# Performance work log

Measured on AMD Instinct MI355X. Metric: run time of the kernel, lower is better.

## Reference

```python
import jax, jax.numpy as jnp
import numpy as np

LOTRI2MAT = np.array([[0, 1, 3], [1, 2, 4], [3, 4, 5]])  # lower-tri 6-vec -> symmetric 3x3
MAT2LOTRI_I = np.array([0, 1, 1, 2, 2, 2])
MAT2LOTRI_J = np.array([0, 0, 1, 0, 1, 2])


def trilinear_warp_border(img, ddf):
    """MONAI Warp(mode='bilinear', padding_mode='border', align_corners=True).
    img: (B,C,H,W,D), ddf: (B,3,H,W,D) displacement in voxel units.
    Samples img at x + ddf(x), clamping coords to the volume (border padding).
    """
    B, C, H, W, D = img.shape
    base = jnp.stack(
        jnp.meshgrid(jnp.arange(H), jnp.arange(W), jnp.arange(D), indexing='ij'),
        axis=0,
    ).astype(img.dtype)  # (3,H,W,D)
    coords = ddf + base[None]  # (B,3,H,W,D)
    x = jnp.clip(coords[:, 0], 0.0, H - 1)
    y = jnp.clip(coords[:, 1], 0.0, W - 1)
    z = jnp.clip(coords[:, 2], 0.0, D - 1)

    x0f, y0f, z0f = jnp.floor(x), jnp.floor(y), jnp.floor(z)
    fx, fy, fz = x - x0f, y - y0f, z - z0f
    x0 = jnp.clip(x0f.astype(jnp.int32), 0, H - 1)
    y0 = jnp.clip(y0f.astype(jnp.int32), 0, W - 1)
    z0 = jnp.clip(z0f.astype(jnp.int32), 0, D - 1)
    x1 = jnp.minimum(x0 + 1, H - 1)
    y1 = jnp.minimum(y0 + 1, W - 1)
    z1 = jnp.minimum(z0 + 1, D - 1)

    def gather(img_b, xi, yi, zi):
        flat = (xi * W + yi) * D + zi  # (H,W,D)
        return img_b.reshape(C, -1)[:, flat.reshape(-1)].reshape(C, H, W, D)

    g = jax.vmap(gather)  # over batch

    out = jnp.zeros_like(img)
    for xi, wx in ((x0, 1.0 - fx), (x1, fx)):
        for yi, wy in ((y0, 1.0 - fy), (y1, fy)):
            for zi, wz in ((z0, 1.0 - fz), (z1, fz)):
                out = out + g(img, xi, yi, zi) * (wx * wy * wz)[:, None]
    return out


def jacobian_of_ddf(ddf):
    """J = I + du/dx via central differences (one-sided at boundaries).
    ddf: (B,3,H,W,D) -> (B,H,W,D,3,3) with J[...,i,j] = d u_i / d x_j + delta_ij."""
    grads = jnp.gradient(ddf, axis=(2, 3, 4))  # list over j of (B,3,H,W,D)
    J = jnp.stack(grads, axis=2)  # (B,3(i),3(j),H,W,D)
    J = J + jnp.eye(3, dtype=ddf.dtype)[None, :, :, None, None, None]
    return jnp.transpose(J, (0, 3, 4, 5, 1, 2))  # (B,H,W,D,3,3)


def setup_inputs() -> dict:
    key = jax.random.key(0)
    k1, k2 = jax.random.split(key)
    dti = jax.random.normal(k1, (2, 6, 64, 64, 64), dtype=jnp.float32)
    ddf = jax.random.normal(k2, (2, 3, 64, 64, 64), dtype=jnp.float32)
    return {"dti": dti, "ddf": ddf}


def reference(dti, ddf):
    b, _, h, w, d = dti.shape
    # 1) trilinear warp of the 6-channel lower-tri DTI
    dti_warped = trilinear_warp_border(dti, ddf)  # (B,6,H,W,D)
    # 2) lower-tri -> full symmetric 3x3, spatial-last
    M = dti_warped[:, LOTRI2MAT]                      # (B,3,3,H,W,D)
    M = jnp.transpose(M, (0, 3, 4, 5, 1, 2))          # (B,H,W,D,3,3)
    # 3) Jacobian of the deformation and its polar-decomposition rotation (finite strain)
    J = jacobian_of_ddf(ddf)                          # (B,H,W,D,3,3)
    U, _, Vh = jnp.linalg.svd(J, full_matrices=False)
    R = jnp.matmul(U, Vh)                             # orthogonal factor of J
    # 4) rotate tensors: R^T M R
    out = jnp.einsum('...ji,...jk,...kl->...il', R, M, R)
    # 5) back to lower-tri channel-first form
    out = jnp.transpose(out, (0, 4, 5, 1, 2, 3))      # (B,3,3,H,W,D)
    return out[:, MAT2LOTRI_I, MAT2LOTRI_J]           # (B,6,H,W,D)
```

## Files before the change

### kernel.cpp

```cpp
#include <hip/hip_runtime.h>

#define NVOX 262144
#define TOTAL (2 * NVOX)

__global__ __launch_bounds__(256)
void warpdti_kernel(const float* __restrict__ dti,
                    const float* __restrict__ ddf,
                    float* __restrict__ out)
{
    const int idx = blockIdx.x * 256 + threadIdx.x;
    const int b = idx >> 18;
    const int r = idx & (NVOX - 1);
    const int x = r >> 12;
    const int y = (r >> 6) & 63;
    const int z = r & 63;

    const float* db = ddf + (size_t)b * 3 * NVOX;

    const float ux = db[r];
    const float uy = db[NVOX + r];
    const float uz = db[2 * NVOX + r];

    const float cx = fminf(fmaxf((float)x + ux, 0.0f), 63.0f);
    const float cy = fminf(fmaxf((float)y + uy, 0.0f), 63.0f);
    const float cz = fminf(fmaxf((float)z + uz, 0.0f), 63.0f);
    const float fx0 = floorf(cx), fy0 = floorf(cy), fz0 = floorf(cz);
    const float fx = cx - fx0, fy = cy - fy0, fz = cz - fz0;
    const int x0 = (int)fx0, y0 = (int)fy0, z0 = (int)fz0;
    const int x1 = min(x0 + 1, 63), y1 = min(y0 + 1, 63), z1 = min(z0 + 1, 63);

    const float gx = 1.0f - fx, gy = 1.0f - fy, gz = 1.0f - fz;
    const float w000 = gx * gy * gz, w001 = gx * gy * fz;
    const float w010 = gx * fy * gz, w011 = gx * fy * fz;
    const float w100 = fx * gy * gz, w101 = fx * gy * fz;
    const float w110 = fx * fy * gz, w111 = fx * fy * fz;

    const int o000 = (x0 * 64 + y0) * 64 + z0, o001 = (x0 * 64 + y0) * 64 + z1;
    const int o010 = (x0 * 64 + y1) * 64 + z0, o011 = (x0 * 64 + y1) * 64 + z1;
    const int o100 = (x1 * 64 + y0) * 64 + z0, o101 = (x1 * 64 + y0) * 64 + z1;
    const int o110 = (x1 * 64 + y1) * 64 + z0, o111 = (x1 * 64 + y1) * 64 + z1;

    const float* tb = dti + (size_t)b * 6 * NVOX;
    float m[6];
#pragma unroll
    for (int c = 0; c < 6; ++c) {
        const float* tc = tb + c * NVOX;
        m[c] = w000 * tc[o000] + w001 * tc[o001]
             + w010 * tc[o010] + w011 * tc[o011]
             + w100 * tc[o100] + w101 * tc[o101]
             + w110 * tc[o110] + w111 * tc[o111];
    }

    const int xm = max(x - 1, 0), xp = min(x + 1, 63);
    const int ym = max(y - 1, 0), yp = min(y + 1, 63);
    const int zm = max(z - 1, 0), zp = min(z + 1, 63);
    const float sx = (xp - xm == 2) ? 0.5f : 1.0f;
    const float sy = (yp - ym == 2) ? 0.5f : 1.0f;
    const float sz = (zp - zm == 2) ? 0.5f : 1.0f;

    const float uc0 = ux, uc1 = uy, uc2 = uz;
    float P[3][3];
#pragma unroll
    for (int i = 0; i < 3; ++i) {
        const float* ui = db + i * NVOX;
        const float ctr = (i == 0) ? uc0 : (i == 1) ? uc1 : uc2;
        P[i][0] = (ui[(xp * 64 + y) * 64 + z] - ui[(xm * 64 + y) * 64 + z]) * sx
                + (i == 0 ? 1.0f : 0.0f);
        P[i][1] = (ui[(x * 64 + yp) * 64 + z] - ui[(x * 64 + ym) * 64 + z]) * sy
                + (i == 1 ? 1.0f : 0.0f);
        P[i][2] = (__shfl(ctr, zp) - __shfl(ctr, zm)) * sz + (i == 2 ? 1.0f : 0.0f);
    }

    float cond_est = 0.0f;
#pragma unroll
    for (int it = 0; it < 8; ++it) {
        const float C00 = P[1][1] * P[2][2] - P[1][2] * P[2][1];
        const float C01 = P[1][2] * P[2][0] - P[1][0] * P[2][2];
        const float C02 = P[1][0] * P[2][1] - P[1][1] * P[2][0];
        const float C10 = P[0][2] * P[2][1] - P[0][1] * P[2][2];
        const float C11 = P[0][0] * P[2][2] - P[0][2] * P[2][0];
        const float C12 = P[0][1] * P[2][0] - P[0][0] * P[2][1];
        const float C20 = P[0][1] * P[1][2] - P[0][2] * P[1][1];
        const float C21 = P[0][2] * P[1][0] - P[0][0] * P[1][2];
        const float C22 = P[0][0] * P[1][1] - P[0][1] * P[1][0];
        const float det = P[0][0] * C00 + P[0][1] * C01 + P[0][2] * C02;

        const float n2 = P[0][0]*P[0][0] + P[0][1]*P[0][1] + P[0][2]*P[0][2]
                       + P[1][0]*P[1][0] + P[1][1]*P[1][1] + P[1][2]*P[1][2]
                       + P[2][0]*P[2][0] + P[2][1]*P[2][1] + P[2][2]*P[2][2];
        const float a2 = C00*C00 + C01*C01 + C02*C02
                       + C10*C10 + C11*C11 + C12*C12
                       + C20*C20 + C21*C21 + C22*C22;

        const float ad = fmaxf(fabsf(det), 1e-30f);
        if (it == 0) cond_est = sqrtf(n2 * a2) / ad;

        const float t  = fmaxf(sqrtf(a2 / n2), 1e-20f);
        const float sg = (det < 0.0f) ? -1.0f : 1.0f;
        const float c1 = 0.5f * sqrtf(t / ad);
        const float c2 = 0.5f * sg / sqrtf(t * ad);

        P[0][0] = c1 * P[0][0] + c2 * C00;  P[0][1] = c1 * P[0][1] + c2 * C01;  P[0][2] = c1 * P[0][2] + c2 * C02;
        P[1][0] = c1 * P[1][0] + c2 * C10;  P[1][1] = c1 * P[1][1] + c2 * C11;  P[1][2] = c1 * P[1][2] + c2 * C12;
        P[2][0] = c1 * P[2][0] + c2 * C20;  P[2][1] = c1 * P[2][1] + c2 * C21;  P[2][2] = c1 * P[2][2] + c2 * C22;
    }

    if (cond_est > 1e4f) {
        double X[3][3];
#pragma unroll
        for (int i = 0; i < 3; ++i) {
            const float* ui = db + i * NVOX;
            X[i][0] = ((double)ui[(xp * 64 + y) * 64 + z]
                     - (double)ui[(xm * 64 + y) * 64 + z]) * (double)sx + (i == 0 ? 1.0 : 0.0);
            X[i][1] = ((double)ui[(x * 64 + yp) * 64 + z]
                     - (double)ui[(x * 64 + ym) * 64 + z]) * (double)sy + (i == 1 ? 1.0 : 0.0);
            X[i][2] = ((double)ui[(x * 64 + y) * 64 + zp]
                     - (double)ui[(x * 64 + y) * 64 + zm]) * (double)sz + (i == 2 ? 1.0 : 0.0);
        }
        for (int it = 0; it < 14; ++it) {
            double mx = 0.0;
#pragma unroll
            for (int i = 0; i < 3; ++i)
#pragma unroll
                for (int j = 0; j < 3; ++j) mx = fmax(mx, fabs(X[i][j]));
            const double s = 1.0 / fmax(mx, 1e-300);
#pragma unroll
            for (int i = 0; i < 3; ++i)
#pragma unroll
                for (int j = 0; j < 3; ++j) X[i][j] *= s;

            const double C00 = X[1][1] * X[2][2] - X[1][2] * X[2][1];
            const double C01 = X[1][2] * X[2][0] - X[1][0] * X[2][2];
            const double C02 = X[1][0] * X[2][1] - X[1][1] * X[2][0];
            const double C10 = X[0][2] * X[2][1] - X[0][1] * X[2][2];
            const double C11 = X[0][0] * X[2][2] - X[0][2] * X[2][0];
            const double C12 = X[0][1] * X[2][0] - X[0][0] * X[2][1];
            const double C20 = X[0][1] * X[1][2] - X[0][2] * X[1][1];
            const double C21 = X[0][2] * X[1][0] - X[0][0] * X[1][2];
            const double C22 = X[0][0] * X[1][1] - X[0][1] * X[1][0];
            const double det = X[0][0] * C00 + X[0][1] * C01 + X[0][2] * C02;

            const double n2 = X[0][0]*X[0][0] + X[0][1]*X[0][1] + X[0][2]*X[0][2]
                            + X[1][0]*X[1][0] + X[1][1]*X[1][1] + X[1][2]*X[1][2]
                            + X[2][0]*X[2][0] + X[2][1]*X[2][1] + X[2][2]*X[2][2];
            const double a2 = C00*C00 + C01*C01 + C02*C02
                            + C10*C10 + C11*C11 + C12*C12
                            + C20*C20 + C21*C21 + C22*C22;

            const double t  = fmax(sqrt(a2 / n2), 1e-150);
            const double ad = fmax(fabs(det), 1e-280);
            const double sg = (det < 0.0) ? -1.0 : 1.0;
            const double c1 = 0.5 * sqrt(t / ad);
            const double c2 = 0.5 * sg / sqrt(t * ad);

            X[0][0] = c1 * X[0][0] + c2 * C00;  X[0][1] = c1 * X[0][1] + c2 * C01;  X[0][2] = c1 * X[0][2] + c2 * C02;
            X[1][0] = c1 * X[1][0] + c2 * C10;  X[1][1] = c1 * X[1][1] + c2 * C11;  X[1][2] = c1 * X[1][2] + c2 * C12;
            X[2][0] = c1 * X[2][0] + c2 * C20;  X[2][1] = c1 * X[2][1] + c2 * C21;  X[2][2] = c1 * X[2][2] + c2 * C22;
        }
#pragma unroll
        for (int i = 0; i < 3; ++i)
#pragma unroll
            for (int j = 0; j < 3; ++j) P[i][j] = (float)X[i][j];
    }

    const float M3[3][3] = {{m[0], m[1], m[3]},
                            {m[1], m[2], m[4]},
                            {m[3], m[4], m[5]}};
    float T[3][3];
#pragma unroll
    for (int i = 0; i < 3; ++i)
#pragma unroll
        for (int j = 0; j < 3; ++j)
            T[i][j] = P[0][i] * M3[0][j] + P[1][i] * M3[1][j] + P[2][i] * M3[2][j];

    float A[3][3];
#pragma unroll
    for (int i = 0; i < 3; ++i)
#pragma unroll
        for (int j = 0; j < 3; ++j)
            A[i][j] = T[i][0] * P[0][j] + T[i][1] * P[1][j] + T[i][2] * P[2][j];

    float* ob = out + (size_t)b * 6 * NVOX;
    ob[0 * NVOX + r] = A[0][0];
    ob[1 * NVOX + r] = A[1][0];
    ob[2 * NVOX + r] = A[1][1];
    ob[3 * NVOX + r] = A[2][0];
    ob[4 * NVOX + r] = A[2][1];
    ob[5 * NVOX + r] = A[2][2];
}

extern "C" void kernel_launch(void* const* d_in, const int* in_sizes, int n_in,
                              void* d_out, int out_size, void* d_ws, size_t ws_size,
                              hipStream_t stream) {
    const float* dti = (const float*)d_in[0];
    const float* ddf = (const float*)d_in[1];
    float* out = (float*)d_out;
    warpdti_kernel<<<TOTAL / 256, 256, 0, stream>>>(dti, ddf, out);
}
```

Measured before the change: 113.7 us.

## Defer ill-conditioned voxels to a double-precision rescue kernel and pair z-loads

The rare fp64 polar-decomposition fallback moves out of the main kernel. Flagged voxels are appended to a workspace list with an atomic counter, and a small second kernel recomputes them in double precision. This removes divergence and register pressure from the main kernel. The trilinear gather also loads the two z-neighbours as one 2-float vector, and the fp32 Newton iterations drop from 8 to 6. In exchange the change adds two extra launches, an atomic per flagged voxel and a cap of 8192 rescued voxels, and the fewer iterations may lose accuracy on moderately conditioned voxels.

```diff
diff --git a/kernel.cpp b/kernel.cpp
--- a/kernel.cpp
+++ b/kernel.cpp
@@ -3,10 +3,17 @@
 #define NVOX 262144
 #define TOTAL (2 * NVOX)
 
+typedef float f2u __attribute__((ext_vector_type(2), aligned(4)));
+
+__global__ void zero_count(int* __restrict__ bad) {
+    if (threadIdx.x == 0) bad[0] = 0;
+}
+
 __global__ __launch_bounds__(256)
-void warpdti_kernel(const float* __restrict__ dti,
-                    const float* __restrict__ ddf,
-                    float* __restrict__ out)
+void warp_main(const float* __restrict__ dti,
+               const float* __restrict__ ddf,
+               float* __restrict__ out,
+               int* __restrict__ bad, int max_bad)
 {
     const int idx = blockIdx.x * 256 + threadIdx.x;
     const int b = idx >> 18;
@@ -27,28 +34,30 @@
     const float fx0 = floorf(cx), fy0 = floorf(cy), fz0 = floorf(cz);
     const float fx = cx - fx0, fy = cy - fy0, fz = cz - fz0;
     const int x0 = (int)fx0, y0 = (int)fy0, z0 = (int)fz0;
-    const int x1 = min(x0 + 1, 63), y1 = min(y0 + 1, 63), z1 = min(z0 + 1, 63);
+    const int x1 = min(x0 + 1, 63), y1 = min(y0 + 1, 63);
 
     const float gx = 1.0f - fx, gy = 1.0f - fy, gz = 1.0f - fz;
-    const float w000 = gx * gy * gz, w001 = gx * gy * fz;
-    const float w010 = gx * fy * gz, w011 = gx * fy * fz;
-    const float w100 = fx * gy * gz, w101 = fx * gy * fz;
-    const float w110 = fx * fy * gz, w111 = fx * fy * fz;
-
-    const int o000 = (x0 * 64 + y0) * 64 + z0, o001 = (x0 * 64 + y0) * 64 + z1;
-    const int o010 = (x0 * 64 + y1) * 64 + z0, o011 = (x0 * 64 + y1) * 64 + z1;
-    const int o100 = (x1 * 64 + y0) * 64 + z0, o101 = (x1 * 64 + y0) * 64 + z1;
-    const int o110 = (x1 * 64 + y1) * 64 + z0, o111 = (x1 * 64 + y1) * 64 + z1;
+    const float q00 = gx * gy, q01 = gx * fy, q10 = fx * gy, q11 = fx * fy;
+
+    const bool ztop = (z0 == 63);
+    const int zb = ztop ? 62 : z0;
+    const int p00 = (x0 * 64 + y0) * 64 + zb, p01 = (x0 * 64 + y1) * 64 + zb;
+    const int p10 = (x1 * 64 + y0) * 64 + zb, p11 = (x1 * 64 + y1) * 64 + zb;
 
     const float* tb = dti + (size_t)b * 6 * NVOX;
     float m[6];
 #pragma unroll
     for (int c = 0; c < 6; ++c) {
         const float* tc = tb + c * NVOX;
-        m[c] = w000 * tc[o000] + w001 * tc[o001]
-             + w010 * tc[o010] + w011 * tc[o011]
-             + w100 * tc[o100] + w101 * tc[o101]
-             + w110 * tc[o110] + w111 * tc[o111];
+        const f2u v00 = *(const f2u*)(tc + p00);
+        const f2u v01 = *(const f2u*)(tc + p01);
+        const f2u v10 = *(const f2u*)(tc + p10);
+        const f2u v11 = *(const f2u*)(tc + p11);
+        const float l00 = (ztop ? v00.y : v00.x) * gz + v00.y * fz;
+        const float l01 = (ztop ? v01.y : v01.x) * gz + v01.y * fz;
+        const float l10 = (ztop ? v10.y : v10.x) * gz + v10.y * fz;
+        const float l11 = (ztop ? v11.y : v11.x) * gz + v11.y * fz;
+        m[c] = q00 * l00 + q01 * l01 + q10 * l10 + q11 * l11;
     }
 
     const int xm = max(x - 1, 0), xp = min(x + 1, 63);
@@ -58,12 +67,11 @@
     const float sy = (yp - ym == 2) ? 0.5f : 1.0f;
     const float sz = (zp - zm == 2) ? 0.5f : 1.0f;
 
-    const float uc0 = ux, uc1 = uy, uc2 = uz;
     float P[3][3];
 #pragma unroll
     for (int i = 0; i < 3; ++i) {
         const float* ui = db + i * NVOX;
-        const float ctr = (i == 0) ? uc0 : (i == 1) ? uc1 : uc2;
+        const float ctr = (i == 0) ? ux : (i == 1) ? uy : uz;
         P[i][0] = (ui[(xp * 64 + y) * 64 + z] - ui[(xm * 64 + y) * 64 + z]) * sx
                 + (i == 0 ? 1.0f : 0.0f);
         P[i][1] = (ui[(x * 64 + yp) * 64 + z] - ui[(x * 64 + ym) * 64 + z]) * sy
@@ -73,7 +81,7 @@
 
     float cond_est = 0.0f;
 #pragma unroll
-    for (int it = 0; it < 8; ++it) {
+    for (int it = 0; it < 6; ++it) {
         const float C00 = P[1][1] * P[2][2] - P[1][2] * P[2][1];
         const float C01 = P[1][2] * P[2][0] - P[1][0] * P[2][2];
         const float C02 = P[1][0] * P[2][1] - P[1][1] * P[2][0];
@@ -105,64 +113,6 @@
         P[2][0] = c1 * P[2][0] + c2 * C20;  P[2][1] = c1 * P[2][1] + c2 * C21;  P[2][2] = c1 * P[2][2] + c2 * C22;
     }
 
-    if (cond_est > 1e4f) {
-        double X[3][3];
-#pragma unroll
-        for (int i = 0; i < 3; ++i) {
-            const float* ui = db + i * NVOX;
-            X[i][0] = ((double)ui[(xp * 64 + y) * 64 + z]
-                     - (double)ui[(xm * 64 + y) * 64 + z]) * (double)sx + (i == 0 ? 1.0 : 0.0);
-            X[i][1] = ((double)ui[(x * 64 + yp) * 64 + z]
-                     - (double)ui[(x * 64 + ym) * 64 + z]) * (double)sy + (i == 1 ? 1.0 : 0.0);
-            X[i][2] = ((double)ui[(x * 64 + y) * 64 + zp]
-                     - (double)ui[(x * 64 + y) * 64 + zm]) * (double)sz + (i == 2 ? 1.0 : 0.0);
-        }
-        for (int it = 0; it < 14; ++it) {
-            double mx = 0.0;
-#pragma unroll
-            for (int i = 0; i < 3; ++i)
-#pragma unroll
-                for (int j = 0; j < 3; ++j) mx = fmax(mx, fabs(X[i][j]));
-            const double s = 1.0 / fmax(mx, 1e-300);
-#pragma unroll
-            for (int i = 0; i < 3; ++i)
-#pragma unroll
-                for (int j = 0; j < 3; ++j) X[i][j] *= s;
-
-            const double C00 = X[1][1] * X[2][2] - X[1][2] * X[2][1];
-            const double C01 = X[1][2] * X[2][0] - X[1][0] * X[2][2];
-            const double C02 = X[1][0] * X[2][1] - X[1][1] * X[2][0];
-            const double C10 = X[0][2] * X[2][1] - X[0][1] * X[2][2];
-            const double C11 = X[0][0] * X[2][2] - X[0][2] * X[2][0];
-            const double C12 = X[0][1] * X[2][0] - X[0][0] * X[2][1];
-            const double C20 = X[0][1] * X[1][2] - X[0][2] * X[1][1];
-            const double C21 = X[0][2] * X[1][0] - X[0][0] * X[1][2];
-            const double C22 = X[0][0] * X[1][1] - X[0][1] * X[1][0];
-            const double det = X[0][0] * C00 + X[0][1] * C01 + X[0][2] * C02;
-
-            const double n2 = X[0][0]*X[0][0] + X[0][1]*X[0][1] + X[0][2]*X[0][2]
-                            + X[1][0]*X[1][0] + X[1][1]*X[1][1] + X[1][2]*X[1][2]
-                            + X[2][0]*X[2][0] + X[2][1]*X[2][1] + X[2][2]*X[2][2];
-            const double a2 = C00*C00 + C01*C01 + C02*C02
-                            + C10*C10 + C11*C11 + C12*C12
-                            + C20*C20 + C21*C21 + C22*C22;
-
-            const double t  = fmax(sqrt(a2 / n2), 1e-150);
-            const double ad = fmax(fabs(det), 1e-280);
-            const double sg = (det < 0.0) ? -1.0 : 1.0;
-            const double c1 = 0.5 * sqrt(t / ad);
-            const double c2 = 0.5 * sg / sqrt(t * ad);
-
-            X[0][0] = c1 * X[0][0] + c2 * C00;  X[0][1] = c1 * X[0][1] + c2 * C01;  X[0][2] = c1 * X[0][2] + c2 * C02;
-            X[1][0] = c1 * X[1][0] + c2 * C10;  X[1][1] = c1 * X[1][1] + c2 * C11;  X[1][2] = c1 * X[1][2] + c2 * C12;
-            X[2][0] = c1 * X[2][0] + c2 * C20;  X[2][1] = c1 * X[2][1] + c2 * C21;  X[2][2] = c1 * X[2][2] + c2 * C22;
-        }
-#pragma unroll
-        for (int i = 0; i < 3; ++i)
-#pragma unroll
-            for (int j = 0; j < 3; ++j) P[i][j] = (float)X[i][j];
-    }
-
     const float M3[3][3] = {{m[0], m[1], m[3]},
                             {m[1], m[2], m[4]},
                             {m[3], m[4], m[5]}};
@@ -187,6 +137,117 @@
     ob[3 * NVOX + r] = A[2][0];
     ob[4 * NVOX + r] = A[2][1];
     ob[5 * NVOX + r] = A[2][2];
+
+    if (cond_est > 1e4f) {
+        const int slot = atomicAdd(bad, 1);
+        if (slot < max_bad) bad[1 + slot] = idx;
+    }
+}
+
+__global__ __launch_bounds__(256)
+void rescue(const float* __restrict__ dti,
+            const float* __restrict__ ddf,
+            float* __restrict__ out,
+            const int* __restrict__ bad, int max_bad)
+{
+    const int n = min(bad[0], max_bad);
+    for (int k = blockIdx.x * 256 + threadIdx.x; k < n; k += 4 * 256) {
+        const int idx = bad[1 + k];
+        const int b = idx >> 18;
+        const int r = idx & (NVOX - 1);
+        const int x = r >> 12;
+        const int y = (r >> 6) & 63;
+        const int z = r & 63;
+
+        const float* db = ddf + (size_t)b * 3 * NVOX;
+
+        const float cx = fminf(fmaxf((float)x + db[r], 0.0f), 63.0f);
+        const float cy = fminf(fmaxf((float)y + db[NVOX + r], 0.0f), 63.0f);
+        const float cz = fminf(fmaxf((float)z + db[2 * NVOX + r], 0.0f), 63.0f);
+        const float fx0 = floorf(cx), fy0 = floorf(cy), fz0 = floorf(cz);
+        const float fx = cx - fx0, fy = cy - fy0, fz = cz - fz0;
+        const int x0 = (int)fx0, y0 = (int)fy0, z0 = (int)fz0;
+        const int x1 = min(x0 + 1, 63), y1 = min(y0 + 1, 63), z1 = min(z0 + 1, 63);
+        const float gx = 1.0f - fx, gy = 1.0f - fy, gz = 1.0f - fz;
+        const float w000 = gx*gy*gz, w001 = gx*gy*fz, w010 = gx*fy*gz, w011 = gx*fy*fz;
+        const float w100 = fx*gy*gz, w101 = fx*gy*fz, w110 = fx*fy*gz, w111 = fx*fy*fz;
+        const int o000 = (x0*64+y0)*64+z0, o001 = (x0*64+y0)*64+z1;
+        const int o010 = (x0*64+y1)*64+z0, o011 = (x0*64+y1)*64+z1;
+        const int o100 = (x1*64+y0)*64+z0, o101 = (x1*64+y0)*64+z1;
+        const int o110 = (x1*64+y1)*64+z0, o111 = (x1*64+y1)*64+z1;
+
+        const float* tb = dti + (size_t)b * 6 * NVOX;
+        float m[6];
+        for (int c = 0; c < 6; ++c) {
+            const float* tc = tb + c * NVOX;
+            m[c] = w000*tc[o000] + w001*tc[o001] + w010*tc[o010] + w011*tc[o011]
+                 + w100*tc[o100] + w101*tc[o101] + w110*tc[o110] + w111*tc[o111];
+        }
+
+        const int xm = max(x-1,0), xp = min(x+1,63);
+        const int ym = max(y-1,0), yp = min(y+1,63);
+        const int zm = max(z-1,0), zp = min(z+1,63);
+        const double sx = (xp-xm==2)?0.5:1.0, sy = (yp-ym==2)?0.5:1.0, sz = (zp-zm==2)?0.5:1.0;
+        double X[3][3];
+        for (int i = 0; i < 3; ++i) {
+            const float* ui = db + i * NVOX;
+            X[i][0] = ((double)ui[(xp*64+y)*64+z] - (double)ui[(xm*64+y)*64+z]) * sx + (i==0?1.0:0.0);
+            X[i][1] = ((double)ui[(x*64+yp)*64+z] - (double)ui[(x*64+ym)*64+z]) * sy + (i==1?1.0:0.0);
+            X[i][2] = ((double)ui[(x*64+y)*64+zp] - (double)ui[(x*64+y)*64+zm]) * sz + (i==2?1.0:0.0);
+        }
+
+        for (int it = 0; it < 14; ++it) {
+            double mx = 0.0;
+            for (int i = 0; i < 3; ++i)
+                for (int j = 0; j < 3; ++j) mx = fmax(mx, fabs(X[i][j]));
+            const double s = 1.0 / fmax(mx, 1e-300);
+            for (int i = 0; i < 3; ++i)
+                for (int j = 0; j < 3; ++j) X[i][j] *= s;
+
+            const double C00 = X[1][1]*X[2][2] - X[1][2]*X[2][1];
+            const double C01 = X[1][2]*X[2][0] - X[1][0]*X[2][2];
+            const double C02 = X[1][0]*X[2][1] - X[1][1]*X[2][0];
+            const double C10 = X[0][2]*X[2][1] - X[0][1]*X[2][2];
+            const double C11 = X[0][0]*X[2][2] - X[0][2]*X[2][0];
+            const double C12 = X[0][1]*X[2][0] - X[0][0]*X[2][1];
+            const double C20 = X[0][1]*X[1][2] - X[0][2]*X[1][1];
+            const double C21 = X[0][2]*X[1][0] - X[0][0]*X[1][2];
+            const double C22 = X[0][0]*X[1][1] - X[0][1]*X[1][0];
+            const double det = X[0][0]*C00 + X[0][1]*C01 + X[0][2]*C02;
+            const double n2 = X[0][0]*X[0][0]+X[0][1]*X[0][1]+X[0][2]*X[0][2]
+                            + X[1][0]*X[1][0]+X[1][1]*X[1][1]+X[1][2]*X[1][2]
+                            + X[2][0]*X[2][0]+X[2][1]*X[2][1]+X[2][2]*X[2][2];
+            const double a2 = C00*C00+C01*C01+C02*C02 + C10*C10+C11*C11+C12*C12
+                            + C20*C20+C21*C21+C22*C22;
+            const double t  = fmax(sqrt(a2 / n2), 1e-150);
+            const double ad = fmax(fabs(det), 1e-280);
+            const double sg = (det < 0.0) ? -1.0 : 1.0;
+            const double c1 = 0.5 * sqrt(t / ad);
+            const double c2 = 0.5 * sg / sqrt(t * ad);
+            X[0][0]=c1*X[0][0]+c2*C00; X[0][1]=c1*X[0][1]+c2*C01; X[0][2]=c1*X[0][2]+c2*C02;
+            X[1][0]=c1*X[1][0]+c2*C10; X[1][1]=c1*X[1][1]+c2*C11; X[1][2]=c1*X[1][2]+c2*C12;
+            X[2][0]=c1*X[2][0]+c2*C20; X[2][1]=c1*X[2][1]+c2*C21; X[2][2]=c1*X[2][2]+c2*C22;
+        }
+
+        const double M3[3][3] = {{(double)m[0], (double)m[1], (double)m[3]},
+                                 {(double)m[1], (double)m[2], (double)m[4]},
+                                 {(double)m[3], (double)m[4], (double)m[5]}};
+        double T[3][3], A[3][3];
+        for (int i = 0; i < 3; ++i)
+            for (int j = 0; j < 3; ++j)
+                T[i][j] = X[0][i]*M3[0][j] + X[1][i]*M3[1][j] + X[2][i]*M3[2][j];
+        for (int i = 0; i < 3; ++i)
+            for (int j = 0; j < 3; ++j)
+                A[i][j] = T[i][0]*X[0][j] + T[i][1]*X[1][j] + T[i][2]*X[2][j];
+
+        float* ob = out + (size_t)b * 6 * NVOX;
+        ob[0 * NVOX + r] = (float)A[0][0];
+        ob[1 * NVOX + r] = (float)A[1][0];
+        ob[2 * NVOX + r] = (float)A[1][1];
+        ob[3 * NVOX + r] = (float)A[2][0];
+        ob[4 * NVOX + r] = (float)A[2][1];
+        ob[5 * NVOX + r] = (float)A[2][2];
+    }
 }
 
 extern "C" void kernel_launch(void* const* d_in, const int* in_sizes, int n_in,
@@ -195,5 +256,10 @@
     const float* dti = (const float*)d_in[0];
     const float* ddf = (const float*)d_in[1];
     float* out = (float*)d_out;
-    warpdti_kernel<<<TOTAL / 256, 256, 0, stream>>>(dti, ddf, out);
-}
+    int* bad = (int*)d_ws;
+    const int max_bad = (int)min((size_t)8192, ws_size / 4 - 1);
+
+    zero_count<<<1, 64, 0, stream>>>(bad);
+    warp_main<<<TOTAL / 256, 256, 0, stream>>>(dti, ddf, out, bad, max_bad);
+    rescue<<<4, 256, 0, stream>>>(dti, ddf, out, bad, max_bad);
+}
```

New measurement: 108.2 us. -4.8%, faster.
